# Performance work log

Hardware: AMD Instinct MI355X
Metric: run time of the kernel (lower is better)

The kernel has to match this reference:

```python
import jax, jax.numpy as jnp
import numpy as np

B, L, D, N, F, V, NL, NS = 2, 1024, 768, 16, 3072, 32000, 4, 3
EPS = 1e-5


def _layernorm(x, g, b):
    m = x.mean(-1, keepdims=True)
    v = ((x - m) ** 2).mean(-1, keepdims=True)
    return (x - m) / jnp.sqrt(v + EPS) * g + b


def _ssm_sublayer(x, cw, A_log, WB, WC, Wdt, dtb, Dsk):
    # x: [B,L,D]; causal depthwise conv, kernel_size=3
    xp = jnp.pad(x, ((0, 0), (2, 0), (0, 0)))
    u = xp[:, :-2] * cw[:, 0] + xp[:, 1:-1] * cw[:, 1] + xp[:, 2:] * cw[:, 2]
    u = jax.nn.silu(u)
    dt = jax.nn.softplus(jnp.einsum('bld,de->ble', u, Wdt) + dtb)   # [B,L,D]
    Bm = jnp.einsum('bld,dn->bln', u, WB)                           # [B,L,N]
    Cm = jnp.einsum('bld,dn->bln', u, WC)                           # [B,L,N]
    A = -jnp.exp(A_log)                                             # [D,N]

    def step(h, t):
        dt_t, u_t, b_t, c_t = t                                     # [B,D],[B,D],[B,N],[B,N]
        h = jnp.exp(dt_t[..., None] * A) * h + (dt_t * u_t)[..., None] * b_t[:, None, :]
        y = jnp.einsum('bdn,bn->bd', h, c_t)
        return h, y

    h0 = jnp.zeros((x.shape[0], x.shape[2], A.shape[1]), x.dtype)
    _, ys = jax.lax.scan(step, h0, (dt.transpose(1, 0, 2), u.transpose(1, 0, 2),
                                    Bm.transpose(1, 0, 2), Cm.transpose(1, 0, 2)))
    return ys.transpose(1, 0, 2) + Dsk * u


def setup_inputs() -> dict:
    key = jax.random.key(0)
    ks = jax.random.split(key, 16)
    g = lambda k, shape, s=0.02: jax.random.normal(k, shape, jnp.float32) * s
    inp = {
        'x': jax.random.randint(ks[0], (B, L), 0, V),
        'emb': g(ks[1], (V, D)),
        'conv_w': g(ks[2], (NL, NS, D, 3), 0.2),
        'A_log': jnp.log(jnp.tile(jnp.arange(1, N + 1, dtype=jnp.float32), (NL, NS, D, 1))),
        'W_B': g(ks[3], (NL, NS, D, N)),
        'W_C': g(ks[4], (NL, NS, D, N)),
        'W_dt': g(ks[5], (NL, NS, D, D)),
        'dt_bias': jnp.full((NL, NS, D), -4.0, jnp.float32),
        'D_skip': jnp.ones((NL, NS, D), jnp.float32),
        'ffn_W1': g(ks[6], (NL, D, F)),
        'ffn_b1': jnp.zeros((NL, F), jnp.float32),
        'ffn_W2': g(ks[7], (NL, F, D)),
        'ffn_b2': jnp.zeros((NL, D), jnp.float32),
        'norm_g': jnp.ones((D,), jnp.float32),
        'norm_b': jnp.zeros((D,), jnp.float32),
        'out_W': g(ks[8], (D, V)),
        'out_b': jnp.zeros((V,), jnp.float32),
    }
    return inp


def reference(x, emb, conv_w, A_log, W_B, W_C, W_dt, dt_bias, D_skip,
              ffn_W1, ffn_b1, ffn_W2, ffn_b2, norm_g, norm_b, out_W, out_b):
    h = emb[x]                                                      # [B,L,D]
    for l in range(NL):
        for s in range(NS):
            h = h + _ssm_sublayer(h, conv_w[l, s], A_log[l, s], W_B[l, s],
                                  W_C[l, s], W_dt[l, s], dt_bias[l, s], D_skip[l, s])
        f = jax.nn.gelu(jnp.einsum('bld,df->blf', h, ffn_W1[l]) + ffn_b1[l], approximate=False)
        h = h + jnp.einsum('blf,fd->bld', f, ffn_W2[l]) + ffn_b2[l]
    h = _layernorm(h, norm_g, norm_b)
    logits = jnp.einsum('bld,dv->blv', h, out_W) + out_b            # [B,L,V]
    return logits
```

## Files before the change

kernel.cpp:

```cpp
#include <hip/hip_runtime.h>
#include <hip/hip_bf16.h>
#include <math.h>

#define BB 2
#define LL 1024
#define DD 768
#define NN 16
#define FF 3072
#define VV 32000
#define NLL 4
#define NSS 3
#define BL (BB*LL)
#define CHK 64
#define CLEN (LL/CHK)

typedef __bf16 bf16x8 __attribute__((ext_vector_type(8)));
typedef float f32x4 __attribute__((ext_vector_type(4)));

typedef __attribute__((address_space(1))) const void gconst_t;
typedef __attribute__((address_space(3))) void lds_t;

__device__ __forceinline__ void g2l16(const void* g, void* l) {
  __builtin_amdgcn_global_load_lds((gconst_t*)g, (lds_t*)l, 16, 0, 0);
}


__global__ __launch_bounds__(256) void k_embed(
    const int* __restrict__ x, const float* __restrict__ emb,
    float* __restrict__ h) {
  int row = blockIdx.x;
  int idx = x[row];
  const float* e = emb + (size_t)idx * DD;
  float* hr = h + (size_t)row * DD;
  int t = threadIdx.x;
  hr[t]       = e[t];
  hr[t + 256] = e[t + 256];
  hr[t + 512] = e[t + 512];
}

__global__ __launch_bounds__(256) void k_conv(
    const float* __restrict__ h, const float* __restrict__ cw,
    __hip_bfloat16* __restrict__ ub) {
  int row = blockIdx.x;
  int l = row & (LL - 1);
  #pragma unroll
  for (int d = threadIdx.x; d < DD; d += 256) {
    float w0 = cw[d * 3 + 0], w1 = cw[d * 3 + 1], w2 = cw[d * 3 + 2];
    float v = h[(size_t)row * DD + d] * w2;
    if (l >= 1) v += h[(size_t)(row - 1) * DD + d] * w1;
    if (l >= 2) v += h[(size_t)(row - 2) * DD + d] * w0;
    float sv = v / (1.f + __expf(-v));
    ub[(size_t)row * DD + d] = __float2bfloat16(sv);
  }
}

__global__ __launch_bounds__(256) void k_layernorm(
    const float* __restrict__ x, const float* __restrict__ g,
    const float* __restrict__ bta, __hip_bfloat16* __restrict__ o) {
  int row = blockIdx.x;
  const float* xr = x + (size_t)row * DD;
  int tid = threadIdx.x;
  float v1 = xr[tid], v2 = xr[tid + 256], v3 = xr[tid + 512];
  float s = v1 + v2 + v3;
  float sq = v1 * v1 + v2 * v2 + v3 * v3;
  #pragma unroll
  for (int m = 1; m < 64; m <<= 1) {
    s  += __shfl_xor(s, m);
    sq += __shfl_xor(sq, m);
  }
  __shared__ float ss[4], sqs[4];
  if ((tid & 63) == 0) { ss[tid >> 6] = s; sqs[tid >> 6] = sq; }
  __syncthreads();
  s  = ss[0] + ss[1] + ss[2] + ss[3];
  sq = sqs[0] + sqs[1] + sqs[2] + sqs[3];
  float mean = s * (1.f / DD);
  float var  = sq * (1.f / DD) - mean * mean;
  float rstd = rsqrtf(var + 1e-5f);
  o[(size_t)row * DD + tid]       = __float2bfloat16((v1 - mean) * rstd * g[tid]       + bta[tid]);
  o[(size_t)row * DD + tid + 256] = __float2bfloat16((v2 - mean) * rstd * g[tid + 256] + bta[tid + 256]);
  o[(size_t)row * DD + tid + 512] = __float2bfloat16((v3 - mean) * rstd * g[tid + 512] + bta[tid + 512]);
}

#define S1 1728
#define S2 1740
#define S3 4044
#define S4 6348
#define SEND 12348

__global__ __launch_bounds__(256) void k_wconv_all(
    const float* __restrict__ Wdt, const float* __restrict__ WB,
    const float* __restrict__ WC, const float* __restrict__ W1,
    const float* __restrict__ W2, const float* __restrict__ Wout,
    __hip_bfloat16* __restrict__ WTdt, __hip_bfloat16* __restrict__ WT1,
    __hip_bfloat16* __restrict__ WT2, __hip_bfloat16* __restrict__ WTlog) {
  __shared__ float T[64][65];
  int bid = blockIdx.x;
  int tid = threadIdx.x;

  if (bid >= S1 && bid < S2) {
    int sub = bid - S1;
    const float* WBp = WB + (size_t)sub * DD * NN;
    const float* WCp = WC + (size_t)sub * DD * NN;
    __hip_bfloat16* dst = WTdt + (size_t)sub * 832 * DD;
    for (int e = tid; e < 64 * DD; e += 256) {
      int r = e / DD, k = e - (e / DD) * DD;
      float v = 0.f;
      if (r < 16)      v = WBp[(size_t)k * NN + r];
      else if (r < 32) v = WCp[(size_t)k * NN + (r - 16)];
      dst[(size_t)(768 + r) * DD + k] = __float2bfloat16(v);
    }
    return;
  }

  const float* W; __hip_bfloat16* WT;
  int K, N, n0, k0;
  if (bid < S1) {
    int sub = bid / 144, t = bid % 144;
    W = Wdt + (size_t)sub * DD * DD; WT = WTdt + (size_t)sub * 832 * DD;
    K = DD; N = DD; n0 = (t % 12) * 64; k0 = (t / 12) * 64;
  } else if (bid < S3) {
    int idx = bid - S2, l = idx / 576, t = idx % 576;
    W = W1 + (size_t)l * DD * FF; WT = WT1 + (size_t)l * FF * DD;
    K = DD; N = FF; n0 = (t % 48) * 64; k0 = (t / 48) * 64;
  } else if (bid < S4) {
    int idx = bid - S3, l = idx / 576, t = idx % 576;
    W = W2 + (size_t)l * FF * DD; WT = WT2 + (size_t)l * DD * FF;
    K = FF; N = DD; n0 = (t % 12) * 64; k0 = (t / 12) * 64;
  } else {
    int t = bid - S4;
    W = Wout; WT = WTlog;
    K = DD; N = VV; n0 = (t % 500) * 64; k0 = (t / 500) * 64;
  }

  int c = tid & 63, r4 = tid >> 6;
  #pragma unroll
  for (int i = 0; i < 16; ++i) {
    int k_l = r4 + i * 4;
    T[k_l][c] = W[(size_t)(k0 + k_l) * N + n0 + c];
  }
  __syncthreads();
  #pragma unroll
  for (int i = 0; i < 16; ++i) {
    int n_l = r4 + i * 4;
    WT[(size_t)(n0 + n_l) * K + k0 + c] = __float2bfloat16(T[c][n_l]);
  }
}

__device__ __forceinline__ float softplus_f(float x) {
  return (x > 20.f) ? x : log1pf(__expf(x));
}
__device__ __forceinline__ float gelu_f(float x) {
  return 0.5f * x * (1.f + erff(x * 0.70710678118654752f));
}

__global__ __launch_bounds__(256) void k_gemm_ffn1(
    const __hip_bfloat16* __restrict__ A, const __hip_bfloat16* __restrict__ BT,
    const float* __restrict__ bias, __hip_bfloat16* __restrict__ Cb) {
  __shared__ __align__(16) __hip_bfloat16 As[128 * 64];
  __shared__ __align__(16) __hip_bfloat16 Bs[128 * 64];
  const int tid = threadIdx.x;
  const int lane = tid & 63, wid = tid >> 6;
  int wg = (blockIdx.x & 7) * 48 + (blockIdx.x >> 3);
  int tn = wg % 24, tm = wg / 24;
  const int bm = tm * 128, bn = tn * 128;
  const int wm = wid >> 1, wn = wid & 1;
  const int sr = lane >> 3;
  const int sk = (lane & 7) * 8;
  const int N = FF, K = DD;

  f32x4 acc[4][4] = {};

  for (int k0 = 0; k0 < K; k0 += 64) {
    __syncthreads();
    #pragma unroll
    for (int cc = 0; cc < 4; ++cc) {
      int ch = wid * 4 + cc;
      int row = ch * 8 + sr;
      g2l16(A  + (size_t)(bm + row) * K + k0 + sk, &As[ch * 512]);
      g2l16(BT + (size_t)(bn + row) * K + k0 + sk, &Bs[ch * 512]);
    }
    __syncthreads();
    #pragma unroll
    for (int kk = 0; kk < 2; ++kk) {
      bf16x8 af[4], bfr[4];
      #pragma unroll
      for (int m = 0; m < 4; ++m)
        af[m] = *(const bf16x8*)&As[(wm * 64 + m * 16 + (lane & 15)) * 64 + kk * 32 + (lane >> 4) * 8];
      #pragma unroll
      for (int n = 0; n < 4; ++n)
        bfr[n] = *(const bf16x8*)&Bs[(wn * 64 + n * 16 + (lane & 15)) * 64 + kk * 32 + (lane >> 4) * 8];
      #pragma unroll
      for (int m = 0; m < 4; ++m)
        #pragma unroll
        for (int n = 0; n < 4; ++n)
          acc[m][n] = __builtin_amdgcn_mfma_f32_16x16x32_bf16(af[m], bfr[n], acc[m][n], 0, 0, 0);
    }
  }

  const int crow0 = (lane >> 4) * 4;
  const int ccol = lane & 15;
  #pragma unroll
  for (int m = 0; m < 4; ++m) {
    #pragma unroll
    for (int n = 0; n < 4; ++n) {
      int col = bn + wn * 64 + n * 16 + ccol;
      float bv = bias[col];
      #pragma unroll
      for (int j = 0; j < 4; ++j) {
        int row = bm + wm * 64 + m * 16 + crow0 + j;
        Cb[(size_t)row * N + col] = __float2bfloat16(gelu_f(acc[m][n][j] + bv));
      }
    }
  }
}

__global__ __launch_bounds__(256) void k_gemm_dtbc64(
    const __hip_bfloat16* __restrict__ A, const __hip_bfloat16* __restrict__ BT,
    const float* __restrict__ dtbias, float* __restrict__ dtb,
    float* __restrict__ Bm, float* __restrict__ Cm) {
  __shared__ __align__(16) __hip_bfloat16 As[64 * 64];
  __shared__ __align__(16) __hip_bfloat16 Bs[64 * 64];
  const int tid = threadIdx.x;
  const int lane = tid & 63, wid = tid >> 6;
  int wg = (blockIdx.x & 7) * 52 + (blockIdx.x >> 3);
  int tn = wg % 13, tm = wg / 13;
  const int bm = tm * 64, bn = tn * 64;
  const int wm = wid >> 1, wn = wid & 1;
  const int sr = lane >> 3;
  const int sk = (lane & 7) * 8;

  f32x4 acc[2][2] = {};

  for (int k0 = 0; k0 < DD; k0 += 64) {
    __syncthreads();
    #pragma unroll
    for (int cc = 0; cc < 2; ++cc) {
      int ch = wid * 2 + cc;
      int row = ch * 8 + sr;
      g2l16(A  + (size_t)(bm + row) * DD + k0 + sk, &As[ch * 512]);
      g2l16(BT + (size_t)(bn + row) * DD + k0 + sk, &Bs[ch * 512]);
    }
    __syncthreads();
    #pragma unroll
    for (int kk = 0; kk < 2; ++kk) {
      bf16x8 af[2], bfr[2];
      #pragma unroll
      for (int m = 0; m < 2; ++m)
        af[m] = *(const bf16x8*)&As[(wm * 32 + m * 16 + (lane & 15)) * 64 + kk * 32 + (lane >> 4) * 8];
      #pragma unroll
      for (int n = 0; n < 2; ++n)
        bfr[n] = *(const bf16x8*)&Bs[(wn * 32 + n * 16 + (lane & 15)) * 64 + kk * 32 + (lane >> 4) * 8];
      #pragma unroll
      for (int m = 0; m < 2; ++m)
        #pragma unroll
        for (int n = 0; n < 2; ++n)
          acc[m][n] = __builtin_amdgcn_mfma_f32_16x16x32_bf16(af[m], bfr[n], acc[m][n], 0, 0, 0);
    }
  }

  const int crow0 = (lane >> 4) * 4;
  const int ccol = lane & 15;
  #pragma unroll
  for (int m = 0; m < 2; ++m) {
    #pragma unroll
    for (int n = 0; n < 2; ++n) {
      int col = bn + wn * 32 + n * 16 + ccol;
      if (col >= 800) continue;
      float bv = (col < DD) ? dtbias[col] : 0.f;
      #pragma unroll
      for (int j = 0; j < 4; ++j) {
        int row = bm + wm * 32 + m * 16 + crow0 + j;
        float v = acc[m][n][j] + bv;
        if (col < DD)       dtb[(size_t)row * DD + col] = softplus_f(v);
        else if (col < 784) Bm[(size_t)row * NN + (col - DD)] = v;
        else                Cm[(size_t)row * NN + (col - 784)] = v;
      }
    }
  }
}

__global__ __launch_bounds__(256) void k_gemm_ffn2s(
    const __hip_bfloat16* __restrict__ A, const __hip_bfloat16* __restrict__ BT,
    const float* __restrict__ bias, float* __restrict__ h) {
  __shared__ __align__(16) __hip_bfloat16 As[64 * 64];
  __shared__ __align__(16) __hip_bfloat16 Bs[64 * 64];
  const int tid = threadIdx.x;
  const int lane = tid & 63, wid = tid >> 6;
  int wg = (blockIdx.x & 7) * 96 + (blockIdx.x >> 3);
  int tile = wg % 384, split = wg / 384;
  int tm = tile % 32, tn = tile / 32;
  const int bm = tm * 64, bn = tn * 64;
  const int wm = wid >> 1, wn = wid & 1;
  const int sr = lane >> 3;
  const int sk = (lane & 7) * 8;
  const int kbeg = split * (FF / 2), kend = kbeg + FF / 2;

  f32x4 acc[2][2] = {};

  for (int k0 = kbeg; k0 < kend; k0 += 64) {
    __syncthreads();
    #pragma unroll
    for (int cc = 0; cc < 2; ++cc) {
      int ch = wid * 2 + cc;
      int row = ch * 8 + sr;
      g2l16(A  + (size_t)(bm + row) * FF + k0 + sk, &As[ch * 512]);
      g2l16(BT + (size_t)(bn + row) * FF + k0 + sk, &Bs[ch * 512]);
    }
    __syncthreads();
    #pragma unroll
    for (int kk = 0; kk < 2; ++kk) {
      bf16x8 af[2], bfr[2];
      #pragma unroll
      for (int m = 0; m < 2; ++m)
        af[m] = *(const bf16x8*)&As[(wm * 32 + m * 16 + (lane & 15)) * 64 + kk * 32 + (lane >> 4) * 8];
      #pragma unroll
      for (int n = 0; n < 2; ++n)
        bfr[n] = *(const bf16x8*)&Bs[(wn * 32 + n * 16 + (lane & 15)) * 64 + kk * 32 + (lane >> 4) * 8];
      #pragma unroll
      for (int m = 0; m < 2; ++m)
        #pragma unroll
        for (int n = 0; n < 2; ++n)
          acc[m][n] = __builtin_amdgcn_mfma_f32_16x16x32_bf16(af[m], bfr[n], acc[m][n], 0, 0, 0);
    }
  }

  const int crow0 = (lane >> 4) * 4;
  const int ccol = lane & 15;
  #pragma unroll
  for (int m = 0; m < 2; ++m) {
    #pragma unroll
    for (int n = 0; n < 2; ++n) {
      int col = bn + wn * 32 + n * 16 + ccol;
      float bv = (split == 0) ? bias[col] : 0.f;
      #pragma unroll
      for (int j = 0; j < 4; ++j) {
        int row = bm + wm * 32 + m * 16 + crow0 + j;
        unsafeAtomicAdd(&h[(size_t)row * DD + col], acc[m][n][j] + bv);
      }
    }
  }
}

__global__ __launch_bounds__(512) void k_gemm_logits2(
    const __hip_bfloat16* __restrict__ A, const __hip_bfloat16* __restrict__ BT,
    const float* __restrict__ bias, float* __restrict__ C, int M, int N, int K) {
  __shared__ __align__(16) __hip_bfloat16 As[256 * 64];
  __shared__ __align__(16) __hip_bfloat16 Bs[128 * 64];
  const int tid = threadIdx.x;
  const int lane = tid & 63, wid = tid >> 6;
  int bid = blockIdx.y * gridDim.x + blockIdx.x;
  int mt = bid & 7, nt = bid >> 3;
  const int bm = mt * 256, bn = nt * 128;
  const int wm = wid >> 1, wn = wid & 1;
  const int sr = lane >> 3;
  const int sk = (lane & 7) * 8;

  f32x4 acc[4][4] = {};

  for (int k0 = 0; k0 < K; k0 += 64) {
    __syncthreads();
    #pragma unroll
    for (int r = 0; r < 4; ++r) {
      int ch = r * 8 + wid;
      int row = ch * 8 + sr;
      g2l16(A + (size_t)(bm + row) * K + k0 + sk, &As[ch * 512]);
    }
    #pragma unroll
    for (int r = 0; r < 2; ++r) {
      int ch = r * 8 + wid;
      int row = ch * 8 + sr;
      g2l16(BT + (size_t)(bn + row) * K + k0 + sk, &Bs[ch * 512]);
    }
    __syncthreads();
    #pragma unroll
    for (int kk = 0; kk < 2; ++kk) {
      bf16x8 af[4], bfr[4];
      #pragma unroll
      for (int m = 0; m < 4; ++m)
        af[m] = *(const bf16x8*)&As[(wm * 64 + m * 16 + (lane & 15)) * 64 + kk * 32 + (lane >> 4) * 8];
      #pragma unroll
      for (int n = 0; n < 4; ++n)
        bfr[n] = *(const bf16x8*)&Bs[(wn * 64 + n * 16 + (lane & 15)) * 64 + kk * 32 + (lane >> 4) * 8];
      #pragma unroll
      for (int m = 0; m < 4; ++m)
        #pragma unroll
        for (int n = 0; n < 4; ++n)
          acc[m][n] = __builtin_amdgcn_mfma_f32_16x16x32_bf16(af[m], bfr[n], acc[m][n], 0, 0, 0);
    }
  }

  const int crow0 = (lane >> 4) * 4;
  const int ccol = lane & 15;
  #pragma unroll
  for (int m = 0; m < 4; ++m) {
    #pragma unroll
    for (int n = 0; n < 4; ++n) {
      int col = bn + wn * 64 + n * 16 + ccol;
      float bv = bias[col];
      #pragma unroll
      for (int j = 0; j < 4; ++j) {
        int row = bm + wm * 64 + m * 16 + crow0 + j;
        C[(size_t)row * N + col] = acc[m][n][j] + bv;
      }
    }
  }
}

__global__ __launch_bounds__(256) void k_scan_a(
    const float* __restrict__ dt, const __hip_bfloat16* __restrict__ ub,
    const float* __restrict__ Bm, const float* __restrict__ A_log,
    float* __restrict__ F, float* __restrict__ SD) {
  int c = blockIdx.x;
  int bd = blockIdx.y;
  int b = bd / 3;
  int d = (bd % 3) * 256 + threadIdx.x;
  float Av[16];
  {
    const float4* al = (const float4*)(A_log + (size_t)d * NN);
    #pragma unroll
    for (int q = 0; q < 4; ++q) {
      float4 v = al[q];
      Av[q * 4 + 0] = -__expf(v.x);
      Av[q * 4 + 1] = -__expf(v.y);
      Av[q * 4 + 2] = -__expf(v.z);
      Av[q * 4 + 3] = -__expf(v.w);
    }
  }
  float h[16];
  #pragma unroll
  for (int n = 0; n < 16; ++n) h[n] = 0.f;
  float sdt = 0.f;
  size_t base = ((size_t)b * LL + (size_t)c * CLEN) * DD + d;
  int row0 = c * CLEN + b * LL;
  #pragma unroll 4
  for (int t = 0; t < CLEN; ++t) {
    float dtv = dt[base + (size_t)t * DD];
    float uv  = __bfloat162float(ub[base + (size_t)t * DD]);
    float Bv[16];
    const float4* bp = (const float4*)(Bm + (size_t)(row0 + t) * NN);
    *(float4*)&Bv[0]  = bp[0];
    *(float4*)&Bv[4]  = bp[1];
    *(float4*)&Bv[8]  = bp[2];
    *(float4*)&Bv[12] = bp[3];
    float du = dtv * uv;
    sdt += dtv;
    #pragma unroll
    for (int n = 0; n < 16; ++n)
      h[n] = __expf(dtv * Av[n]) * h[n] + du * Bv[n];
  }
  float* fo = F + (((size_t)c * BB + b) * DD + d) * NN;
  #pragma unroll
  for (int q = 0; q < 4; ++q)
    *(float4*)&fo[q * 4] = *(float4*)&h[q * 4];
  SD[((size_t)c * BB + b) * DD + d] = sdt;
}

__global__ __launch_bounds__(256) void k_scan_b(
    const float* __restrict__ F, const float* __restrict__ SD,
    const float* __restrict__ A_log, float* __restrict__ Hinit) {
  __shared__ float Ls[64 * 17];
  __shared__ float Ho[64 * 17];
  __shared__ float Ss[64];
  int bd = blockIdx.x;
  int b = bd / DD, d = bd % DD;
  int tid = threadIdx.x;
  {
    int c = tid >> 2, q = tid & 3;
    float4 v = *(const float4*)(F + (((size_t)c * BB + b) * DD + d) * NN + q * 4);
    Ls[c * 17 + q * 4 + 0] = v.x;
    Ls[c * 17 + q * 4 + 1] = v.y;
    Ls[c * 17 + q * 4 + 2] = v.z;
    Ls[c * 17 + q * 4 + 3] = v.w;
  }
  if (tid < 64) Ss[tid] = SD[((size_t)tid * BB + b) * DD + d];
  __syncthreads();
  int lane = tid & 63, w = tid >> 6;
  #pragma unroll
  for (int r = 0; r < 4; ++r) {
    int n = w * 4 + r;
    float Av = -__expf(A_log[(size_t)d * NN + n]);
    float Fv = Ls[lane * 17 + n];
    float Dv = __expf(Ss[lane] * Av);
    #pragma unroll
    for (int s = 1; s < 64; s <<= 1) {
      float Fp = __shfl_up(Fv, s);
      float Dp = __shfl_up(Dv, s);
      float nF = Fv + Dv * Fp;
      float nD = Dv * Dp;
      Fv = (lane >= s) ? nF : Fv;
      Dv = (lane >= s) ? nD : Dv;
    }
    float Hi = __shfl_up(Fv, 1);
    if (lane == 0) Hi = 0.f;
    Ho[lane * 17 + n] = Hi;
  }
  __syncthreads();
  {
    int c = tid >> 2, q = tid & 3;
    float4 v;
    v.x = Ho[c * 17 + q * 4 + 0];
    v.y = Ho[c * 17 + q * 4 + 1];
    v.z = Ho[c * 17 + q * 4 + 2];
    v.w = Ho[c * 17 + q * 4 + 3];
    *(float4*)(Hinit + (((size_t)c * BB + b) * DD + d) * NN + q * 4) = v;
  }
}

__global__ __launch_bounds__(256) void k_scan_c(
    const float* __restrict__ dt, const __hip_bfloat16* __restrict__ ub,
    const float* __restrict__ Bm, const float* __restrict__ Cm,
    const float* __restrict__ A_log, const float* __restrict__ Dsk,
    const float* __restrict__ Hinit, float* __restrict__ hres,
    __hip_bfloat16* __restrict__ hb) {
  int c = blockIdx.x;
  int bd = blockIdx.y;
  int b = bd / 3;
  int d = (bd % 3) * 256 + threadIdx.x;
  float Av[16];
  {
    const float4* al = (const float4*)(A_log + (size_t)d * NN);
    #pragma unroll
    for (int q = 0; q < 4; ++q) {
      float4 v = al[q];
      Av[q * 4 + 0] = -__expf(v.x);
      Av[q * 4 + 1] = -__expf(v.y);
      Av[q * 4 + 2] = -__expf(v.z);
      Av[q * 4 + 3] = -__expf(v.w);
    }
  }
  float h[16];
  {
    const float4* hi = (const float4*)(Hinit + (((size_t)c * BB + b) * DD + d) * NN);
    #pragma unroll
    for (int q = 0; q < 4; ++q)
      *(float4*)&h[q * 4] = hi[q];
  }
  float dskip = Dsk[d];
  size_t base = ((size_t)b * LL + (size_t)c * CLEN) * DD + d;
  int row0 = c * CLEN + b * LL;
  #pragma unroll 4
  for (int t = 0; t < CLEN; ++t) {
    float dtv = dt[base + (size_t)t * DD];
    float uv  = __bfloat162float(ub[base + (size_t)t * DD]);
    float Bv[16], Cv[16];
    const float4* bp = (const float4*)(Bm + (size_t)(row0 + t) * NN);
    const float4* cp = (const float4*)(Cm + (size_t)(row0 + t) * NN);
    *(float4*)&Bv[0]  = bp[0];
    *(float4*)&Bv[4]  = bp[1];
    *(float4*)&Bv[8]  = bp[2];
    *(float4*)&Bv[12] = bp[3];
    *(float4*)&Cv[0]  = cp[0];
    *(float4*)&Cv[4]  = cp[1];
    *(float4*)&Cv[8]  = cp[2];
    *(float4*)&Cv[12] = cp[3];
    float du = dtv * uv;
    float y = 0.f;
    #pragma unroll
    for (int n = 0; n < 16; ++n) {
      h[n] = __expf(dtv * Av[n]) * h[n] + du * Bv[n];
      y += h[n] * Cv[n];
    }
    float nh = hres[base + (size_t)t * DD] + y + dskip * uv;
    hres[base + (size_t)t * DD] = nh;
    hb[base + (size_t)t * DD] = __float2bfloat16(nh);
  }
}

extern "C" void kernel_launch(void* const* d_in, const int* in_sizes, int n_in,
                              void* d_out, int out_size, void* d_ws, size_t ws_size,
                              hipStream_t stream) {
  const int*   x     = (const int*)d_in[0];
  const float* emb   = (const float*)d_in[1];
  const float* convw = (const float*)d_in[2];
  const float* A_log = (const float*)d_in[3];
  const float* W_B   = (const float*)d_in[4];
  const float* W_C   = (const float*)d_in[5];
  const float* W_dt  = (const float*)d_in[6];
  const float* dt_b  = (const float*)d_in[7];
  const float* D_sk  = (const float*)d_in[8];
  const float* W1    = (const float*)d_in[9];
  const float* b1    = (const float*)d_in[10];
  const float* W2    = (const float*)d_in[11];
  const float* b2    = (const float*)d_in[12];
  const float* ng    = (const float*)d_in[13];
  const float* nb    = (const float*)d_in[14];
  const float* Wout  = (const float*)d_in[15];
  const float* bout  = (const float*)d_in[16];
  float* out = (float*)d_out;

  __hip_bfloat16* WTdt = (__hip_bfloat16*)d_out;
  __hip_bfloat16* WT1  = WTdt + (size_t)12 * 832 * DD;
  __hip_bfloat16* WT2  = WT1  + (size_t)NLL * FF * DD;

  char* p = (char*)d_ws;
  auto alloc = [&](size_t bytes) { char* r = p; p += (bytes + 255) & ~(size_t)255; return r; };
  float* h    = (float*)alloc((size_t)BL * DD * 4);
  float* dtb  = (float*)alloc((size_t)BL * DD * 4);
  float* Bm   = (float*)alloc((size_t)BL * NN * 4);
  float* Cm   = (float*)alloc((size_t)BL * NN * 4);
  float* F    = (float*)alloc((size_t)CHK * BB * DD * NN * 4);
  float* SD   = (float*)alloc((size_t)CHK * BB * DD * 4);
  float* Hini = (float*)alloc((size_t)CHK * BB * DD * NN * 4);
  __hip_bfloat16* ub    = (__hip_bfloat16*)alloc((size_t)BL * DD * 2);
  __hip_bfloat16* hb    = (__hip_bfloat16*)alloc((size_t)BL * DD * 2);
  __hip_bfloat16* fb    = (__hip_bfloat16*)alloc((size_t)BL * FF * 2);
  __hip_bfloat16* lnb   = (__hip_bfloat16*)alloc((size_t)BL * DD * 2);
  __hip_bfloat16* WTlog = (__hip_bfloat16*)alloc((size_t)VV * DD * 2);

  k_wconv_all<<<SEND, 256, 0, stream>>>(
      W_dt, W_B, W_C, W1, W2, Wout, WTdt, WT1, WT2, WTlog);
  k_embed<<<BL, 256, 0, stream>>>(x, emb, h);

  for (int l = 0; l < NLL; ++l) {
    for (int s = 0; s < NSS; ++s) {
      int ls = l * NSS + s;
      k_conv<<<BL, 256, 0, stream>>>(h, convw + (size_t)ls * DD * 3, ub);
      k_gemm_dtbc64<<<416, 256, 0, stream>>>(
          ub, WTdt + (size_t)ls * 832 * DD, dt_b + (size_t)ls * DD, dtb, Bm, Cm);
      k_scan_a<<<dim3(CHK, 6), 256, 0, stream>>>(
          dtb, ub, Bm, A_log + (size_t)ls * DD * NN, F, SD);
      k_scan_b<<<BB * DD, 256, 0, stream>>>(
          F, SD, A_log + (size_t)ls * DD * NN, Hini);
      k_scan_c<<<dim3(CHK, 6), 256, 0, stream>>>(
          dtb, ub, Bm, Cm, A_log + (size_t)ls * DD * NN, D_sk + (size_t)ls * DD,
          Hini, h, hb);
    }
    k_gemm_ffn1<<<384, 256, 0, stream>>>(
        hb, WT1 + (size_t)l * FF * DD, b1 + (size_t)l * FF, fb);
    k_gemm_ffn2s<<<768, 256, 0, stream>>>(
        fb, WT2 + (size_t)l * DD * FF, b2 + (size_t)l * DD, h);
  }

  k_layernorm<<<BL, 256, 0, stream>>>(h, ng, nb, lnb);
  k_gemm_logits2<<<dim3(VV / 128, BL / 256), 512, 0, stream>>>(
      lnb, WTlog, bout, out, BL, VV, DD);
}
```

Baseline: 1.215 ms.

## Double-buffer LDS tiles in all MFMA GEMMs to overlap loads with compute

```diff
diff --git a/kernel.cpp b/kernel.cpp
--- a/kernel.cpp
+++ b/kernel.cpp
@@ -22,6 +22,9 @@
 
 __device__ __forceinline__ void g2l16(const void* g, void* l) {
   __builtin_amdgcn_global_load_lds((gconst_t*)g, (lds_t*)l, 16, 0, 0);
+}
+__device__ __forceinline__ void vm_drain() {
+  asm volatile("s_waitcnt vmcnt(0)" ::: "memory");
 }
 
 
@@ -156,8 +159,8 @@
 __global__ __launch_bounds__(256) void k_gemm_ffn1(
     const __hip_bfloat16* __restrict__ A, const __hip_bfloat16* __restrict__ BT,
     const float* __restrict__ bias, __hip_bfloat16* __restrict__ Cb) {
-  __shared__ __align__(16) __hip_bfloat16 As[128 * 64];
-  __shared__ __align__(16) __hip_bfloat16 Bs[128 * 64];
+  __shared__ __align__(16) __hip_bfloat16 As[2][128 * 64];
+  __shared__ __align__(16) __hip_bfloat16 Bs[2][128 * 64];
   const int tid = threadIdx.x;
   const int lane = tid & 63, wid = tid >> 6;
   int wg = (blockIdx.x & 7) * 48 + (blockIdx.x >> 3);
@@ -168,33 +171,41 @@
   const int sk = (lane & 7) * 8;
   const int N = FF, K = DD;
 
-  f32x4 acc[4][4] = {};
-
-  for (int k0 = 0; k0 < K; k0 += 64) {
-    __syncthreads();
+  auto stage = [&](int buf, int k0) {
     #pragma unroll
     for (int cc = 0; cc < 4; ++cc) {
       int ch = wid * 4 + cc;
       int row = ch * 8 + sr;
-      g2l16(A  + (size_t)(bm + row) * K + k0 + sk, &As[ch * 512]);
-      g2l16(BT + (size_t)(bn + row) * K + k0 + sk, &Bs[ch * 512]);
-    }
-    __syncthreads();
+      g2l16(A  + (size_t)(bm + row) * K + k0 + sk, &As[buf][ch * 512]);
+      g2l16(BT + (size_t)(bn + row) * K + k0 + sk, &Bs[buf][ch * 512]);
+    }
+  };
+
+  f32x4 acc[4][4] = {};
+  stage(0, 0);
+  vm_drain();
+  __syncthreads();
+  const int NT = K / 64;
+  for (int kt = 0; kt < NT; ++kt) {
+    int cur = kt & 1;
+    if (kt + 1 < NT) stage(cur ^ 1, (kt + 1) * 64);
     #pragma unroll
     for (int kk = 0; kk < 2; ++kk) {
       bf16x8 af[4], bfr[4];
       #pragma unroll
       for (int m = 0; m < 4; ++m)
-        af[m] = *(const bf16x8*)&As[(wm * 64 + m * 16 + (lane & 15)) * 64 + kk * 32 + (lane >> 4) * 8];
+        af[m] = *(const bf16x8*)&As[cur][(wm * 64 + m * 16 + (lane & 15)) * 64 + kk * 32 + (lane >> 4) * 8];
       #pragma unroll
       for (int n = 0; n < 4; ++n)
-        bfr[n] = *(const bf16x8*)&Bs[(wn * 64 + n * 16 + (lane & 15)) * 64 + kk * 32 + (lane >> 4) * 8];
+        bfr[n] = *(const bf16x8*)&Bs[cur][(wn * 64 + n * 16 + (lane & 15)) * 64 + kk * 32 + (lane >> 4) * 8];
       #pragma unroll
       for (int m = 0; m < 4; ++m)
         #pragma unroll
         for (int n = 0; n < 4; ++n)
           acc[m][n] = __builtin_amdgcn_mfma_f32_16x16x32_bf16(af[m], bfr[n], acc[m][n], 0, 0, 0);
     }
+    vm_drain();
+    __syncthreads();
   }
 
   const int crow0 = (lane >> 4) * 4;
@@ -218,8 +229,8 @@
     const __hip_bfloat16* __restrict__ A, const __hip_bfloat16* __restrict__ BT,
     const float* __restrict__ dtbias, float* __restrict__ dtb,
     float* __restrict__ Bm, float* __restrict__ Cm) {
-  __shared__ __align__(16) __hip_bfloat16 As[64 * 64];
-  __shared__ __align__(16) __hip_bfloat16 Bs[64 * 64];
+  __shared__ __align__(16) __hip_bfloat16 As[2][64 * 64];
+  __shared__ __align__(16) __hip_bfloat16 Bs[2][64 * 64];
   const int tid = threadIdx.x;
   const int lane = tid & 63, wid = tid >> 6;
   int wg = (blockIdx.x & 7) * 52 + (blockIdx.x >> 3);
@@ -229,33 +240,41 @@
   const int sr = lane >> 3;
   const int sk = (lane & 7) * 8;
 
-  f32x4 acc[2][2] = {};
-
-  for (int k0 = 0; k0 < DD; k0 += 64) {
-    __syncthreads();
+  auto stage = [&](int buf, int k0) {
     #pragma unroll
     for (int cc = 0; cc < 2; ++cc) {
       int ch = wid * 2 + cc;
       int row = ch * 8 + sr;
-      g2l16(A  + (size_t)(bm + row) * DD + k0 + sk, &As[ch * 512]);
-      g2l16(BT + (size_t)(bn + row) * DD + k0 + sk, &Bs[ch * 512]);
-    }
-    __syncthreads();
+      g2l16(A  + (size_t)(bm + row) * DD + k0 + sk, &As[buf][ch * 512]);
+      g2l16(BT + (size_t)(bn + row) * DD + k0 + sk, &Bs[buf][ch * 512]);
+    }
+  };
+
+  f32x4 acc[2][2] = {};
+  stage(0, 0);
+  vm_drain();
+  __syncthreads();
+  const int NT = DD / 64;
+  for (int kt = 0; kt < NT; ++kt) {
+    int cur = kt & 1;
+    if (kt + 1 < NT) stage(cur ^ 1, (kt + 1) * 64);
     #pragma unroll
     for (int kk = 0; kk < 2; ++kk) {
       bf16x8 af[2], bfr[2];
       #pragma unroll
       for (int m = 0; m < 2; ++m)
-        af[m] = *(const bf16x8*)&As[(wm * 32 + m * 16 + (lane & 15)) * 64 + kk * 32 + (lane >> 4) * 8];
+        af[m] = *(const bf16x8*)&As[cur][(wm * 32 + m * 16 + (lane & 15)) * 64 + kk * 32 + (lane >> 4) * 8];
       #pragma unroll
       for (int n = 0; n < 2; ++n)
-        bfr[n] = *(const bf16x8*)&Bs[(wn * 32 + n * 16 + (lane & 15)) * 64 + kk * 32 + (lane >> 4) * 8];
+        bfr[n] = *(const bf16x8*)&Bs[cur][(wn * 32 + n * 16 + (lane & 15)) * 64 + kk * 32 + (lane >> 4) * 8];
       #pragma unroll
       for (int m = 0; m < 2; ++m)
         #pragma unroll
         for (int n = 0; n < 2; ++n)
           acc[m][n] = __builtin_amdgcn_mfma_f32_16x16x32_bf16(af[m], bfr[n], acc[m][n], 0, 0, 0);
     }
+    vm_drain();
+    __syncthreads();
   }
 
   const int crow0 = (lane >> 4) * 4;
@@ -282,8 +301,8 @@
 __global__ __launch_bounds__(256) void k_gemm_ffn2s(
     const __hip_bfloat16* __restrict__ A, const __hip_bfloat16* __restrict__ BT,
     const float* __restrict__ bias, float* __restrict__ h) {
-  __shared__ __align__(16) __hip_bfloat16 As[64 * 64];
-  __shared__ __align__(16) __hip_bfloat16 Bs[64 * 64];
+  __shared__ __align__(16) __hip_bfloat16 As[2][64 * 64];
+  __shared__ __align__(16) __hip_bfloat16 Bs[2][64 * 64];
   const int tid = threadIdx.x;
   const int lane = tid & 63, wid = tid >> 6;
   int wg = (blockIdx.x & 7) * 96 + (blockIdx.x >> 3);
@@ -293,35 +312,43 @@
   const int wm = wid >> 1, wn = wid & 1;
   const int sr = lane >> 3;
   const int sk = (lane & 7) * 8;
-  const int kbeg = split * (FF / 2), kend = kbeg + FF / 2;
-
-  f32x4 acc[2][2] = {};
-
-  for (int k0 = kbeg; k0 < kend; k0 += 64) {
-    __syncthreads();
+  const int kbeg = split * (FF / 2);
+
+  auto stage = [&](int buf, int k0) {
     #pragma unroll
     for (int cc = 0; cc < 2; ++cc) {
       int ch = wid * 2 + cc;
       int row = ch * 8 + sr;
-      g2l16(A  + (size_t)(bm + row) * FF + k0 + sk, &As[ch * 512]);
-      g2l16(BT + (size_t)(bn + row) * FF + k0 + sk, &Bs[ch * 512]);
-    }
-    __syncthreads();
+      g2l16(A  + (size_t)(bm + row) * FF + k0 + sk, &As[buf][ch * 512]);
+      g2l16(BT + (size_t)(bn + row) * FF + k0 + sk, &Bs[buf][ch * 512]);
+    }
+  };
+
+  f32x4 acc[2][2] = {};
+  stage(0, kbeg);
+  vm_drain();
+  __syncthreads();
+  const int NT = (FF / 2) / 64;
+  for (int kt = 0; kt < NT; ++kt) {
+    int cur = kt & 1;
+    if (kt + 1 < NT) stage(cur ^ 1, kbeg + (kt + 1) * 64);
     #pragma unroll
     for (int kk = 0; kk < 2; ++kk) {
       bf16x8 af[2], bfr[2];
       #pragma unroll
       for (int m = 0; m < 2; ++m)
-        af[m] = *(const bf16x8*)&As[(wm * 32 + m * 16 + (lane & 15)) * 64 + kk * 32 + (lane >> 4) * 8];
+        af[m] = *(const bf16x8*)&As[cur][(wm * 32 + m * 16 + (lane & 15)) * 64 + kk * 32 + (lane >> 4) * 8];
       #pragma unroll
       for (int n = 0; n < 2; ++n)
-        bfr[n] = *(const bf16x8*)&Bs[(wn * 32 + n * 16 + (lane & 15)) * 64 + kk * 32 + (lane >> 4) * 8];
+        bfr[n] = *(const bf16x8*)&Bs[cur][(wn * 32 + n * 16 + (lane & 15)) * 64 + kk * 32 + (lane >> 4) * 8];
       #pragma unroll
       for (int m = 0; m < 2; ++m)
         #pragma unroll
         for (int n = 0; n < 2; ++n)
           acc[m][n] = __builtin_amdgcn_mfma_f32_16x16x32_bf16(af[m], bfr[n], acc[m][n], 0, 0, 0);
     }
+    vm_drain();
+    __syncthreads();
   }
 
   const int crow0 = (lane >> 4) * 4;
@@ -344,8 +371,8 @@
 __global__ __launch_bounds__(512) void k_gemm_logits2(
     const __hip_bfloat16* __restrict__ A, const __hip_bfloat16* __restrict__ BT,
     const float* __restrict__ bias, float* __restrict__ C, int M, int N, int K) {
-  __shared__ __align__(16) __hip_bfloat16 As[256 * 64];
-  __shared__ __align__(16) __hip_bfloat16 Bs[128 * 64];
+  __shared__ __align__(16) __hip_bfloat16 As[2][256 * 64];
+  __shared__ __align__(16) __hip_bfloat16 Bs[2][128 * 64];
   const int tid = threadIdx.x;
   const int lane = tid & 63, wid = tid >> 6;
   int bid = blockIdx.y * gridDim.x + blockIdx.x;
@@ -355,38 +382,46 @@
   const int sr = lane >> 3;
   const int sk = (lane & 7) * 8;
 
-  f32x4 acc[4][4] = {};
-
-  for (int k0 = 0; k0 < K; k0 += 64) {
-    __syncthreads();
+  auto stage = [&](int buf, int k0) {
     #pragma unroll
     for (int r = 0; r < 4; ++r) {
       int ch = r * 8 + wid;
       int row = ch * 8 + sr;
-      g2l16(A + (size_t)(bm + row) * K + k0 + sk, &As[ch * 512]);
+      g2l16(A + (size_t)(bm + row) * K + k0 + sk, &As[buf][ch * 512]);
     }
     #pragma unroll
     for (int r = 0; r < 2; ++r) {
       int ch = r * 8 + wid;
       int row = ch * 8 + sr;
-      g2l16(BT + (size_t)(bn + row) * K + k0 + sk, &Bs[ch * 512]);
-    }
-    __syncthreads();
+      g2l16(BT + (size_t)(bn + row) * K + k0 + sk, &Bs[buf][ch * 512]);
+    }
+  };
+
+  f32x4 acc[4][4] = {};
+  stage(0, 0);
+  vm_drain();
+  __syncthreads();
+  const int NT = K / 64;
+  for (int kt = 0; kt < NT; ++kt) {
+    int cur = kt & 1;
+    if (kt + 1 < NT) stage(cur ^ 1, (kt + 1) * 64);
     #pragma unroll
     for (int kk = 0; kk < 2; ++kk) {
       bf16x8 af[4], bfr[4];
       #pragma unroll
       for (int m = 0; m < 4; ++m)
-        af[m] = *(const bf16x8*)&As[(wm * 64 + m * 16 + (lane & 15)) * 64 + kk * 32 + (lane >> 4) * 8];
+        af[m] = *(const bf16x8*)&As[cur][(wm * 64 + m * 16 + (lane & 15)) * 64 + kk * 32 + (lane >> 4) * 8];
       #pragma unroll
       for (int n = 0; n < 4; ++n)
-        bfr[n] = *(const bf16x8*)&Bs[(wn * 64 + n * 16 + (lane & 15)) * 64 + kk * 32 + (lane >> 4) * 8];
+        bfr[n] = *(const bf16x8*)&Bs[cur][(wn * 64 + n * 16 + (lane & 15)) * 64 + kk * 32 + (lane >> 4) * 8];
       #pragma unroll
       for (int m = 0; m < 4; ++m)
         #pragma unroll
         for (int n = 0; n < 4; ++n)
           acc[m][n] = __builtin_amdgcn_mfma_f32_16x16x32_bf16(af[m], bfr[n], acc[m][n], 0, 0, 0);
     }
+    vm_drain();
+    __syncthreads();
   }
 
   const int crow0 = (lane >> 4) * 4;
@@ -400,7 +435,7 @@
       #pragma unroll
       for (int j = 0; j < 4; ++j) {
         int row = bm + wm * 64 + m * 16 + crow0 + j;
-        C[(size_t)row * N + col] = acc[m][n][j] + bv;
+        __builtin_nontemporal_store(acc[m][n][j] + bv, &C[(size_t)row * N + col]);
       }
     }
   }
```

Measured after the change: 1.331 ms. +9.5%, slower.
